# Optimization experiments

Measured on AMD Instinct MI355X. Metric: run time of the kernel, lower is better.

Reference implementation:

```python
import jax, jax.numpy as jnp
import numpy as np
from jax import lax

B, N, C, HEADS = 4096, 49, 256, 8
HD = C // HEADS
SCALE = HD ** -0.5
BRANCHES = [(1, 0), (2, 0), (3, 1), (4, 2)]  # (dilation, padding) for d1..d4


def setup_inputs() -> dict:
    key = jax.random.key(0)
    ks = jax.random.split(key, 24)
    f = lambda i, shape: jax.random.normal(ks[i], shape, dtype=jnp.float32) * 0.05
    inp = {"x": jax.random.normal(ks[0], (B, N, C), dtype=jnp.float32)}
    inp["wq"] = f(1, (C, C)); inp["bq"] = f(2, (C,))
    for j in range(4):
        inp[f"wd{j+1}"] = f(3 + 4 * j, (C, 1, 3, 3))
        inp[f"bd{j+1}"] = f(4 + 4 * j, (C,))
        inp[f"wp{j+1}"] = f(5 + 4 * j, (2 * C, C))
        inp[f"bp{j+1}"] = f(6 + 4 * j, (2 * C,))
    inp["wproj"] = f(19, (C, C)); inp["bproj"] = f(20, (C,))
    return inp


def _branch(x4, wd, bd, wp, bp, dil, pad):
    # depthwise 3x3 stride-2 dilated conv
    d = lax.conv_general_dilated(
        x4, wd, window_strides=(2, 2), padding=[(pad, pad), (pad, pad)],
        rhs_dilation=(dil, dil), dimension_numbers=('NCHW', 'OIHW', 'NCHW'),
        feature_group_count=C) + bd[None, :, None, None]
    # pointwise 1x1 conv C -> 2C
    p = jnp.einsum('oc,bchw->bohw', wp, d) + bp[None, :, None, None]
    # replicate torch's reshape(B,C,-1).permute(0,2,1).reshape(B,-1,2,h,hd).permute(2,0,3,1,4)
    p = p.reshape(B, C, -1).transpose(0, 2, 1)
    p = p.reshape(B, -1, 2, HEADS, HD).transpose(2, 0, 3, 1, 4)
    return p[0], p[1]  # k, v: (B, HEADS, hw, HD)


def _forward(x, wq, bq, wd1, bd1, wp1, bp1, wd2, bd2, wp2, bp2,
             wd3, bd3, wp3, bp3, wd4, bd4, wp4, bp4, wproj, bproj):
    H = int(N ** 0.5)
    x4 = x.transpose(0, 2, 1).reshape(B, C, H, H)
    params = [(wd1, bd1, wp1, bp1), (wd2, bd2, wp2, bp2),
              (wd3, bd3, wp3, bp3), (wd4, bd4, wp4, bp4)]
    ks_, vs_ = [], []
    for (wd, bd, wp, bp), (dil, pad) in zip(params, BRANCHES):
        k_, v_ = _branch(x4, wd, bd, wp, bp, dil, pad)
        ks_.append(k_); vs_.append(v_)
    k = jnp.concatenate(ks_, axis=2)  # (B, HEADS, 21, HD)
    v = jnp.concatenate(vs_, axis=2)
    q = (jnp.einsum('bnc,oc->bno', x, wq) + bq)
    q = q.reshape(B, N, HEADS, HD).transpose(0, 2, 1, 3) * SCALE  # (B, H, N, HD)
    attn = jax.nn.softmax(jnp.einsum('bhnd,bhmd->bhnm', q, k), axis=-1)
    out = jnp.einsum('bhnm,bhmd->bhnd', attn, v)
    out = out.transpose(0, 2, 1, 3).reshape(B, N, C)
    return jnp.einsum('bnc,oc->bno', out, wproj) + bproj


def reference(x, wq, bq, wd1, bd1, wp1, bp1, wd2, bd2, wp2, bp2,
              wd3, bd3, wp3, bp3, wd4, bd4, wp4, bp4, wproj, bproj):
    return _forward(x, wq, bq, wd1, bd1, wp1, bp1, wd2, bd2, wp2, bp2,
                    wd3, bd3, wp3, bp3, wd4, bd4, wp4, bp4, wproj, bproj)
```

## Files before the change

### kernel.cpp

```cpp
#include <hip/hip_runtime.h>
#include <stdint.h>

typedef __attribute__((ext_vector_type(8))) short bf16x8;
typedef __attribute__((ext_vector_type(8))) unsigned short u16x8;
typedef __attribute__((ext_vector_type(4))) float f32x4;

#define DEV __device__ __forceinline__

constexpr size_t WQ_PK    = 0;
constexpr size_t WPROJ_PK = 65536;
constexpr size_t WP_PK    = 131072;
constexpr size_t KVBUF    = 655360;

constexpr float SCALE_Q = 0.17677669529663687f;

DEV uint16_t f2bf(float f){
  uint32_t u = __builtin_bit_cast(uint32_t, f);
  u += 0x7fffu + ((u >> 16) & 1u);
  return (uint16_t)(u >> 16);
}

DEV u16x8 extract_par(u16x8 a, u16x8 b, uint32_t sel){
  union U { u16x8 v; uint32_t d[4]; } A, B, R;
  A.v = a; B.v = b;
  R.d[0] = __builtin_amdgcn_perm(A.d[1], A.d[0], sel);
  R.d[1] = __builtin_amdgcn_perm(A.d[3], A.d[2], sel);
  R.d[2] = __builtin_amdgcn_perm(B.d[1], B.d[0], sel);
  R.d[3] = __builtin_amdgcn_perm(B.d[3], B.d[2], sel);
  return R.v;
}

__global__ __launch_bounds__(256) void k_prepack(
    const float* __restrict__ wq,  const float* __restrict__ wp1,
    const float* __restrict__ wp2, const float* __restrict__ wp3,
    const float* __restrict__ wp4, const float* __restrict__ wproj,
    uint16_t* __restrict__ ws)
{
  int f = blockIdx.x * 256 + threadIdx.x;
  const float* src; uint16_t* dst; int g;
  if (f < 8192)       { src = wq;    dst = ws + WQ_PK;    g = f; }
  else if (f < 16384) { src = wproj; dst = ws + WPROJ_PK; g = f - 8192; }
  else {
    int j = (f - 16384) >> 14;
    src = j == 0 ? wp1 : j == 1 ? wp2 : j == 2 ? wp3 : wp4;
    dst = ws + WP_PK + (size_t)j * 131072;
    g = (f - 16384) & 16383;
  }
  int l = g & 63, kt = (g >> 6) & 7, nt = g >> 9;
  int n  = nt * 16 + (l & 15);
  int k0 = kt * 32 + (l >> 4) * 8;
  const float* s = src + (size_t)n * 256 + k0;
  u16x8 v;
  #pragma unroll
  for (int j = 0; j < 8; ++j) v[j] = f2bf(s[j]);
  *reinterpret_cast<u16x8*>(dst + (size_t)g * 8) = v;
}

__global__ __launch_bounds__(512, 2) void k_kv(
    const float* __restrict__ x,
    const float* __restrict__ wd1, const float* __restrict__ bd1, const float* __restrict__ bp1,
    const float* __restrict__ wd2, const float* __restrict__ bd2, const float* __restrict__ bp2,
    const float* __restrict__ wd3, const float* __restrict__ bd3, const float* __restrict__ bp3,
    const float* __restrict__ wd4, const float* __restrict__ bd4, const float* __restrict__ bp4,
    const uint16_t* __restrict__ ws, uint16_t* __restrict__ kvbuf)
{
  extern __shared__ char smem[];
  const int t = threadIdx.x, lane = t & 63, w = t >> 6;
  const int b0 = blockIdx.x * 8;

  constexpr int DILA[4] = {1,2,3,4}, PADA[4] = {0,0,1,2}, OWA[4] = {3,2,2,2};
  constexpr int HWA[4]  = {9,4,4,4}, OFFA[4] = {0,9,13,17}, MTA[4] = {5,2,2,2};

  {
    const int c = t & 255, half = t >> 8;
    for (int pass = 0; pass < 4; ++pass){
      const int bh = pass * 2 + half;
      float xr[49];
      #pragma unroll
      for (int p = 0; p < 49; ++p)
        xr[p] = x[((size_t)(b0 + bh) * 49 + p) * 256 + c];
      #pragma unroll
      for (int j = 0; j < 4; ++j){
        const float* wdp = j==0?wd1:j==1?wd2:j==2?wd3:wd4;
        const float* bdp = j==0?bd1:j==1?bd2:j==2?bd3:bd4;
        float wv[9];
        #pragma unroll
        for (int q = 0; q < 9; ++q) wv[q] = wdp[c * 9 + q];
        const float bdv = bdp[c];
        #pragma unroll
        for (int oy = 0; oy < OWA[j]; ++oy)
        #pragma unroll
        for (int ox = 0; ox < OWA[j]; ++ox){
          float acc = bdv;
          #pragma unroll
          for (int ky = 0; ky < 3; ++ky){
            const int yy = oy * 2 - PADA[j] + ky * DILA[j];
            if (yy < 0 || yy > 6) continue;
            #pragma unroll
            for (int kx = 0; kx < 3; ++kx){
              const int xx = ox * 2 - PADA[j] + kx * DILA[j];
              if (xx < 0 || xx > 6) continue;
              acc += xr[yy * 7 + xx] * wv[ky * 3 + kx];
            }
          }
          const int row = bh * 21 + OFFA[j] + oy * OWA[j] + ox;
          *reinterpret_cast<uint16_t*>(smem + ((row * 512 + c * 2) ^ ((row & 7) << 4))) = f2bf(acc);
        }
      }
    }
  }
  __syncthreads();

  #pragma unroll
  for (int j = 0; j < 4; ++j){
    const uint16_t* pk = ws + WP_PK + (size_t)j * 131072;
    const float* bpp = j==0?bp1:j==1?bp2:j==2?bp3:bp4;
    const int hw = HWA[j], off = OFFA[j], MV = hw * 8;
    float bpv[4];
    #pragma unroll
    for (int nt = 0; nt < 4; ++nt) bpv[nt] = bpp[w * 64 + nt * 16 + (lane & 15)];
    for (int mt = 0; mt < MTA[j]; ++mt){
      f32x4 acc[4] = {};
      const int mrow = mt * 16 + (lane & 15);
      const bool av = mrow < MV;
      const int bh = mrow / hw, s = mrow - bh * hw;
      const int arow = bh * 21 + off + s;
      const int abase = arow * 512 + (lane >> 4) * 16;
      #pragma unroll
      for (int kt = 0; kt < 8; ++kt){
        bf16x8 a = {};
        if (av) a = *reinterpret_cast<const bf16x8*>(smem + ((abase + kt * 64) ^ ((arow & 7) << 4)));
        #pragma unroll
        for (int nt = 0; nt < 4; ++nt){
          const int ntg = w * 4 + nt;
          bf16x8 bfr = *reinterpret_cast<const bf16x8*>(pk + (size_t)((ntg * 8 + kt) * 64 + lane) * 8);
          acc[nt] = __builtin_amdgcn_mfma_f32_16x16x32_bf16(a, bfr, acc[nt], 0, 0, 0);
        }
      }
      const int mr2 = mt * 16 + (lane >> 4) * 4;
      #pragma unroll
      for (int i = 0; i < 4; ++i){
        const int m = mr2 + i;
        if (m >= MV) continue;
        const int bh2 = m / hw, s2 = m - bh2 * hw;
        const size_t grow = ((size_t)(b0 + bh2) * 21 + off + s2) * 512;
        #pragma unroll
        for (int nt = 0; nt < 4; ++nt)
          kvbuf[grow + w * 64 + nt * 16 + (lane & 15)] = f2bf(acc[nt][i] + bpv[nt]);
      }
    }
  }
}

__global__ __launch_bounds__(512, 4) void k_attn(
    const float* __restrict__ x, const float* __restrict__ bq,
    const float* __restrict__ bproj, const uint16_t* __restrict__ ws,
    float* __restrict__ out)
{
  extern __shared__ char smem[];
  constexpr int OSB = 32768;
  const int t = threadIdx.x, lane = t & 63, w = t >> 6;
  const size_t b = blockIdx.x;
  const uint16_t* wq_pk    = ws + WQ_PK;
  const uint16_t* wproj_pk = ws + WPROJ_PK;
  const uint16_t* kvbuf    = ws + KVBUF;

  {
    const int r = t >> 3, c0 = (t & 7) * 32;
    u16x8 vv[4] = {};
    if (r < 49){
      const float* src = x + (b * 49 + r) * 256 + c0;
      #pragma unroll
      for (int jj = 0; jj < 4; ++jj){
        f32x4 f0 = *reinterpret_cast<const f32x4*>(src + jj * 8);
        f32x4 f1 = *reinterpret_cast<const f32x4*>(src + jj * 8 + 4);
        union { u16x8 v; uint32_t d[4]; } R;
        asm("v_cvt_pk_bf16_f32 %0, %1, %2" : "=v"(R.d[0]) : "v"(f0[0]), "v"(f0[1]));
        asm("v_cvt_pk_bf16_f32 %0, %1, %2" : "=v"(R.d[1]) : "v"(f0[2]), "v"(f0[3]));
        asm("v_cvt_pk_bf16_f32 %0, %1, %2" : "=v"(R.d[2]) : "v"(f1[0]), "v"(f1[1]));
        asm("v_cvt_pk_bf16_f32 %0, %1, %2" : "=v"(R.d[3]) : "v"(f1[2]), "v"(f1[3]));
        vv[jj] = R.v;
      }
    }
    #pragma unroll
    for (int jj = 0; jj < 4; ++jj)
      *reinterpret_cast<u16x8*>(smem + ((r * 512 + c0 * 2 + jj * 16) ^ ((r & 7) << 4))) = vv[jj];
  }

  const int sh4 = t >> 7, m = (t >> 2) & 31, dch = (t & 3) * 8;
  const bool mv = m < 21;
  uint32_t selK = 0x05040100u, selV = 0x05040100u;
  const uint16_t *rk = kvbuf, *rv = kvbuf;
  if (mv){
    int off, hw;
    if (m < 9)       { off = 0;  hw = 9; }
    else if (m < 13) { off = 9;  hw = 4; }
    else if (m < 17) { off = 13; hw = 4; }
    else             { off = 17; hw = 4; }
    const int ml = m - off;
    const int c2k = 2 * ml,     ek = c2k >= hw ? 1 : 0, sk = c2k - ek * hw;
    const int c2v = 2 * ml + 1, ev = c2v >= hw ? 1 : 0, sv = c2v - ev * hw;
    selK = ek ? 0x07060302u : 0x05040100u;
    selV = ev ? 0x07060302u : 0x05040100u;
    const int o0 = 2 * (sh4 * 32 + dch);
    rk = kvbuf + (b * 21 + off + sk) * 512 + o0;
    rv = kvbuf + (b * 21 + off + sv) * 512 + o0;
  }
  u16x8 L0 = {}, L1 = {}, L2 = {}, L3 = {};
  if (mv){
    L0 = *reinterpret_cast<const u16x8*>(rk);
    L1 = *reinterpret_cast<const u16x8*>(rk + 8);
    L2 = *reinterpret_cast<const u16x8*>(rv);
    L3 = *reinterpret_cast<const u16x8*>(rv + 8);
  }
  __syncthreads();

  f32x4 qacc[4][2] = {};
  #pragma unroll 2
  for (int kt = 0; kt < 8; ++kt){
    bf16x8 a[4];
    #pragma unroll
    for (int mt = 0; mt < 4; ++mt){
      const int row = mt * 16 + (lane & 15);
      a[mt] = *reinterpret_cast<const bf16x8*>(smem + ((row * 512 + kt * 64 + (lane >> 4) * 16) ^ ((row & 7) << 4)));
    }
    #pragma unroll
    for (int nt = 0; nt < 2; ++nt){
      bf16x8 bfr = *reinterpret_cast<const bf16x8*>(wq_pk + (size_t)(((w * 2 + nt) * 8 + kt) * 64 + lane) * 8);
      #pragma unroll
      for (int mt = 0; mt < 4; ++mt)
        qacc[mt][nt] = __builtin_amdgcn_mfma_f32_16x16x32_bf16(a[mt], bfr, qacc[mt][nt], 0, 0, 0);
    }
  }
  #pragma unroll
  for (int nt = 0; nt < 2; ++nt){
    const int col = w * 32 + nt * 16 + (lane & 15);
    const float bqv = bq[col];
    #pragma unroll
    for (int mt = 0; mt < 4; ++mt)
      #pragma unroll
      for (int i = 0; i < 4; ++i){
        const int row = mt * 16 + (lane >> 4) * 4 + i;
        *reinterpret_cast<uint16_t*>(smem + OSB + ((row * 512 + col * 2) ^ ((row & 7) << 4)))
          = f2bf((qacc[mt][nt][i] + bqv) * SCALE_Q);
      }
  }
  __syncthreads();

  for (int p = 0; p < 2; ++p){
    {
      u16x8 kf = extract_par(L0, L1, selK);
      u16x8 vf = extract_par(L2, L3, selV);
      *reinterpret_cast<u16x8*>(smem + sh4 * 2048 + ((m * 64 + dch * 2) ^ ((m & 7) << 4))) = kf;
      #pragma unroll
      for (int jj = 0; jj < 8; ++jj){
        const int d = dch + jj;
        *reinterpret_cast<uint16_t*>(smem + 8192 + sh4 * 2048 + ((d * 64 + m * 2) ^ ((d & 7) << 4))) = vf[jj];
      }
      if (p == 0 && mv){
        L0 = *reinterpret_cast<const u16x8*>(rk + 256);
        L1 = *reinterpret_cast<const u16x8*>(rk + 264);
        L2 = *reinterpret_cast<const u16x8*>(rv + 256);
        L3 = *reinterpret_cast<const u16x8*>(rv + 264);
      }
    }
    __syncthreads();

    const int h4 = w >> 1, wh = w & 1;
    const int hcol = (p * 4 + h4) * 64;
    const int pabase = 16384 + h4 * 4096;

    bf16x8 bk[2];
    #pragma unroll
    for (int nt = 0; nt < 2; ++nt){
      const int m0 = nt * 16 + (lane & 15);
      bk[nt] = *reinterpret_cast<const bf16x8*>(smem + h4 * 2048 + ((m0 * 64 + (lane >> 4) * 16) ^ ((m0 & 7) << 4)));
    }
    f32x4 sacc[2][2];
    #pragma unroll
    for (int mt = 0; mt < 2; ++mt){
      const int row = wh * 32 + mt * 16 + (lane & 15);
      bf16x8 aq = *reinterpret_cast<const bf16x8*>(smem + OSB + ((row * 512 + hcol + (lane >> 4) * 16) ^ ((row & 7) << 4)));
      #pragma unroll
      for (int nt = 0; nt < 2; ++nt){
        f32x4 z = {};
        sacc[mt][nt] = __builtin_amdgcn_mfma_f32_16x16x32_bf16(aq, bk[nt], z, 0, 0, 0);
      }
    }
    const bool ok1 = (lane & 15) < 5;
    #pragma unroll
    for (int mt = 0; mt < 2; ++mt)
      #pragma unroll
      for (int i = 0; i < 4; ++i){
        const float s0 = sacc[mt][0][i];
        const float s1 = sacc[mt][1][i];
        float mx = fmaxf(s0, ok1 ? s1 : -3.0e38f);
        #pragma unroll
        for (int dd = 1; dd < 16; dd <<= 1) mx = fmaxf(mx, __shfl_xor(mx, dd));
        const float e0 = __expf(s0 - mx);
        const float e1 = ok1 ? __expf(s1 - mx) : 0.f;
        float sm = e0 + e1;
        #pragma unroll
        for (int dd = 1; dd < 16; dd <<= 1) sm += __shfl_xor(sm, dd);
        const float inv = 1.0f / sm;
        const int pr = wh * 32 + mt * 16 + (lane >> 4) * 4 + i;
        const int c0 = lane & 15;
        *reinterpret_cast<uint16_t*>(smem + pabase + ((pr * 64 + c0 * 2) ^ ((pr & 7) << 4))) = f2bf(e0 * inv);
        *reinterpret_cast<uint16_t*>(smem + pabase + ((pr * 64 + (c0 + 16) * 2) ^ ((pr & 7) << 4))) = f2bf(e1 * inv);
      }
    f32x4 oacc[2][2];
    #pragma unroll
    for (int mt = 0; mt < 2; ++mt){
      const int pr = wh * 32 + mt * 16 + (lane & 15);
      bf16x8 ap = *reinterpret_cast<const bf16x8*>(smem + pabase + ((pr * 64 + (lane >> 4) * 16) ^ ((pr & 7) << 4)));
      #pragma unroll
      for (int nt = 0; nt < 2; ++nt){
        const int d0 = nt * 16 + (lane & 15);
        bf16x8 bv = *reinterpret_cast<const bf16x8*>(smem + 8192 + h4 * 2048 + ((d0 * 64 + (lane >> 4) * 16) ^ ((d0 & 7) << 4)));
        f32x4 z = {};
        oacc[mt][nt] = __builtin_amdgcn_mfma_f32_16x16x32_bf16(ap, bv, z, 0, 0, 0);
      }
    }
    #pragma unroll
    for (int mt = 0; mt < 2; ++mt)
      #pragma unroll
      for (int nt = 0; nt < 2; ++nt)
        #pragma unroll
        for (int i = 0; i < 4; ++i){
          const int row = wh * 32 + mt * 16 + (lane >> 4) * 4 + i;
          const int colb = hcol + (nt * 16 + (lane & 15)) * 2;
          *reinterpret_cast<uint16_t*>(smem + OSB + ((row * 512 + colb) ^ ((row & 7) << 4))) = f2bf(oacc[mt][nt][i]);
        }
    __syncthreads();
  }

  f32x4 pacc[4][2] = {};
  #pragma unroll 2
  for (int kt = 0; kt < 8; ++kt){
    bf16x8 a[4];
    #pragma unroll
    for (int mt = 0; mt < 4; ++mt){
      const int row = mt * 16 + (lane & 15);
      a[mt] = *reinterpret_cast<const bf16x8*>(smem + OSB + ((row * 512 + kt * 64 + (lane >> 4) * 16) ^ ((row & 7) << 4)));
    }
    #pragma unroll
    for (int nt = 0; nt < 2; ++nt){
      bf16x8 bfr = *reinterpret_cast<const bf16x8*>(wproj_pk + (size_t)(((w * 2 + nt) * 8 + kt) * 64 + lane) * 8);
      #pragma unroll
      for (int mt = 0; mt < 4; ++mt)
        pacc[mt][nt] = __builtin_amdgcn_mfma_f32_16x16x32_bf16(a[mt], bfr, pacc[mt][nt], 0, 0, 0);
    }
  }
  #pragma unroll
  for (int nt = 0; nt < 2; ++nt){
    const int col = w * 32 + nt * 16 + (lane & 15);
    const float bpv = bproj[col];
    #pragma unroll
    for (int mt = 0; mt < 4; ++mt)
      #pragma unroll
      for (int i = 0; i < 4; ++i){
        const int n = mt * 16 + (lane >> 4) * 4 + i;
        if (n < 49)
          out[(b * 49 + n) * 256 + col] = pacc[mt][nt][i] + bpv;
      }
  }
}

extern "C" void kernel_launch(void* const* d_in, const int* in_sizes, int n_in,
                              void* d_out, int out_size, void* d_ws, size_t ws_size,
                              hipStream_t stream)
{
  const float* x     = (const float*)d_in[0];
  const float* wq    = (const float*)d_in[1];
  const float* bq    = (const float*)d_in[2];
  const float* wd1   = (const float*)d_in[3];
  const float* bd1   = (const float*)d_in[4];
  const float* wp1   = (const float*)d_in[5];
  const float* bp1   = (const float*)d_in[6];
  const float* wd2   = (const float*)d_in[7];
  const float* bd2   = (const float*)d_in[8];
  const float* wp2   = (const float*)d_in[9];
  const float* bp2   = (const float*)d_in[10];
  const float* wd3   = (const float*)d_in[11];
  const float* bd3   = (const float*)d_in[12];
  const float* wp3   = (const float*)d_in[13];
  const float* bp3   = (const float*)d_in[14];
  const float* wd4   = (const float*)d_in[15];
  const float* bd4   = (const float*)d_in[16];
  const float* wp4   = (const float*)d_in[17];
  const float* bp4   = (const float*)d_in[18];
  const float* wproj = (const float*)d_in[19];
  const float* bproj = (const float*)d_in[20];
  uint16_t* ws = (uint16_t*)d_ws;
  float* out = (float*)d_out;

  k_prepack<<<320, 256, 0, stream>>>(wq, wp1, wp2, wp3, wp4, wproj, ws);
  k_kv<<<512, 512, 86016, stream>>>(x, wd1, bd1, bp1, wd2, bd2, bp2,
                                    wd3, bd3, bp3, wd4, bd4, bp4,
                                    ws, ws + KVBUF);
  k_attn<<<4096, 512, 65536, stream>>>(x, bq, bproj, ws, out);
}
```

Measured before the change: 277.5 us.

## Swap MFMA operand roles so outputs land channel-contiguous for vector stores

Transposes the three GEMMs (pointwise KV, Q projection, output projection): weights become the A operand and activations the B operand. Each lane's four accumulator values then sit on consecutive output channels, so results are written as packed bf16 pairs or float4 vectors instead of scattered scalar stores. Bias is loaded as a float4 per lane, and the x staging into shared memory is moved after the KV global loads so more loads are in flight. The intent is to cut store instruction count and uncoalesced global writes, at the cost of retouching index math in several stages.

```diff
diff --git a/kernel.cpp b/kernel.cpp
--- a/kernel.cpp
+++ b/kernel.cpp
@@ -4,6 +4,7 @@
 typedef __attribute__((ext_vector_type(8))) short bf16x8;
 typedef __attribute__((ext_vector_type(8))) unsigned short u16x8;
 typedef __attribute__((ext_vector_type(4))) float f32x4;
+typedef __attribute__((ext_vector_type(2))) uint32_t u32x2;
 
 #define DEV __device__ __forceinline__
 
@@ -12,12 +13,18 @@
 constexpr size_t WP_PK    = 131072;
 constexpr size_t KVBUF    = 655360;
 
-constexpr float SCALE_Q = 0.17677669529663687f;
+constexpr float SCALE_Q  = 0.17677669529663687f;
 
 DEV uint16_t f2bf(float f){
   uint32_t u = __builtin_bit_cast(uint32_t, f);
   u += 0x7fffu + ((u >> 16) & 1u);
   return (uint16_t)(u >> 16);
+}
+
+DEV uint32_t cvtpk(float a, float b){
+  uint32_t r;
+  asm("v_cvt_pk_bf16_f32 %0, %1, %2" : "=v"(r) : "v"(a), "v"(b));
+  return r;
 }
 
 DEV u16x8 extract_par(u16x8 a, u16x8 b, uint32_t sel){
@@ -66,6 +73,7 @@
 {
   extern __shared__ char smem[];
   const int t = threadIdx.x, lane = t & 63, w = t >> 6;
+  const int q4 = lane >> 4, c15 = lane & 15;
   const int b0 = blockIdx.x * 8;
 
   constexpr int DILA[4] = {1,2,3,4}, PADA[4] = {0,0,1,2}, OWA[4] = {3,2,2,2};
@@ -115,38 +123,34 @@
   for (int j = 0; j < 4; ++j){
     const uint16_t* pk = ws + WP_PK + (size_t)j * 131072;
     const float* bpp = j==0?bp1:j==1?bp2:j==2?bp3:bp4;
-    const int hw = HWA[j], off = OFFA[j], MV = hw * 8;
-    float bpv[4];
-    #pragma unroll
-    for (int nt = 0; nt < 4; ++nt) bpv[nt] = bpp[w * 64 + nt * 16 + (lane & 15)];
-    for (int mt = 0; mt < MTA[j]; ++mt){
+    const int hw = HWA[j], off = OFFA[j], MV = hw * 8, ST = MTA[j];
+    for (int st = 0; st < ST; ++st){
+      const int sl = st * 16 + c15;
+      const bool sv = sl < MV;
+      const int svc = sv ? sl : 0;
+      const int bh = svc / hw, sp = svc - bh * hw;
+      const int arow = bh * 21 + off + sp;
       f32x4 acc[4] = {};
-      const int mrow = mt * 16 + (lane & 15);
-      const bool av = mrow < MV;
-      const int bh = mrow / hw, s = mrow - bh * hw;
-      const int arow = bh * 21 + off + s;
-      const int abase = arow * 512 + (lane >> 4) * 16;
       #pragma unroll
       for (int kt = 0; kt < 8; ++kt){
-        bf16x8 a = {};
-        if (av) a = *reinterpret_cast<const bf16x8*>(smem + ((abase + kt * 64) ^ ((arow & 7) << 4)));
-        #pragma unroll
-        for (int nt = 0; nt < 4; ++nt){
-          const int ntg = w * 4 + nt;
-          bf16x8 bfr = *reinterpret_cast<const bf16x8*>(pk + (size_t)((ntg * 8 + kt) * 64 + lane) * 8);
-          acc[nt] = __builtin_amdgcn_mfma_f32_16x16x32_bf16(a, bfr, acc[nt], 0, 0, 0);
+        bf16x8 bfr = *reinterpret_cast<const bf16x8*>(smem + ((arow * 512 + kt * 64 + q4 * 16) ^ ((arow & 7) << 4)));
+        #pragma unroll
+        for (int ot = 0; ot < 4; ++ot){
+          bf16x8 aw = *reinterpret_cast<const bf16x8*>(pk + (size_t)(((w * 4 + ot) * 8 + kt) * 64 + lane) * 8);
+          acc[ot] = __builtin_amdgcn_mfma_f32_16x16x32_bf16(aw, bfr, acc[ot], 0, 0, 0);
         }
       }
-      const int mr2 = mt * 16 + (lane >> 4) * 4;
-      #pragma unroll
-      for (int i = 0; i < 4; ++i){
-        const int m = mr2 + i;
-        if (m >= MV) continue;
-        const int bh2 = m / hw, s2 = m - bh2 * hw;
-        const size_t grow = ((size_t)(b0 + bh2) * 21 + off + s2) * 512;
-        #pragma unroll
-        for (int nt = 0; nt < 4; ++nt)
-          kvbuf[grow + w * 64 + nt * 16 + (lane & 15)] = f2bf(acc[nt][i] + bpv[nt]);
+      if (sv){
+        const size_t grow = ((size_t)(b0 + bh) * 21 + off + sp) * 512;
+        #pragma unroll
+        for (int ot = 0; ot < 4; ++ot){
+          const int ob = w * 64 + ot * 16 + q4 * 4;
+          const f32x4 vb = *reinterpret_cast<const f32x4*>(bpp + ob);
+          u32x2 pkv;
+          pkv[0] = cvtpk(acc[ot][0] + vb[0], acc[ot][1] + vb[1]);
+          pkv[1] = cvtpk(acc[ot][2] + vb[2], acc[ot][3] + vb[3]);
+          *reinterpret_cast<u32x2*>(kvbuf + grow + ob) = pkv;
+        }
       }
     }
   }
@@ -160,32 +164,11 @@
   extern __shared__ char smem[];
   constexpr int OSB = 32768;
   const int t = threadIdx.x, lane = t & 63, w = t >> 6;
+  const int q4 = lane >> 4, c15 = lane & 15;
   const size_t b = blockIdx.x;
   const uint16_t* wq_pk    = ws + WQ_PK;
   const uint16_t* wproj_pk = ws + WPROJ_PK;
   const uint16_t* kvbuf    = ws + KVBUF;
-
-  {
-    const int r = t >> 3, c0 = (t & 7) * 32;
-    u16x8 vv[4] = {};
-    if (r < 49){
-      const float* src = x + (b * 49 + r) * 256 + c0;
-      #pragma unroll
-      for (int jj = 0; jj < 4; ++jj){
-        f32x4 f0 = *reinterpret_cast<const f32x4*>(src + jj * 8);
-        f32x4 f1 = *reinterpret_cast<const f32x4*>(src + jj * 8 + 4);
-        union { u16x8 v; uint32_t d[4]; } R;
-        asm("v_cvt_pk_bf16_f32 %0, %1, %2" : "=v"(R.d[0]) : "v"(f0[0]), "v"(f0[1]));
-        asm("v_cvt_pk_bf16_f32 %0, %1, %2" : "=v"(R.d[1]) : "v"(f0[2]), "v"(f0[3]));
-        asm("v_cvt_pk_bf16_f32 %0, %1, %2" : "=v"(R.d[2]) : "v"(f1[0]), "v"(f1[1]));
-        asm("v_cvt_pk_bf16_f32 %0, %1, %2" : "=v"(R.d[3]) : "v"(f1[2]), "v"(f1[3]));
-        vv[jj] = R.v;
-      }
-    }
-    #pragma unroll
-    for (int jj = 0; jj < 4; ++jj)
-      *reinterpret_cast<u16x8*>(smem + ((r * 512 + c0 * 2 + jj * 16) ^ ((r & 7) << 4))) = vv[jj];
-  }
 
   const int sh4 = t >> 7, m = (t >> 2) & 31, dch = (t & 3) * 8;
   const bool mv = m < 21;
@@ -213,37 +196,59 @@
     L2 = *reinterpret_cast<const u16x8*>(rv);
     L3 = *reinterpret_cast<const u16x8*>(rv + 8);
   }
+
+  {
+    const int r = t >> 3, c0 = (t & 7) * 32;
+    u16x8 vv[4] = {};
+    if (r < 49){
+      const float* src = x + (b * 49 + r) * 256 + c0;
+      #pragma unroll
+      for (int jj = 0; jj < 4; ++jj){
+        f32x4 f0 = *reinterpret_cast<const f32x4*>(src + jj * 8);
+        f32x4 f1 = *reinterpret_cast<const f32x4*>(src + jj * 8 + 4);
+        union { u16x8 v; uint32_t d[4]; } R;
+        R.d[0] = cvtpk(f0[0], f0[1]);
+        R.d[1] = cvtpk(f0[2], f0[3]);
+        R.d[2] = cvtpk(f1[0], f1[1]);
+        R.d[3] = cvtpk(f1[2], f1[3]);
+        vv[jj] = R.v;
+      }
+    }
+    #pragma unroll
+    for (int jj = 0; jj < 4; ++jj)
+      *reinterpret_cast<u16x8*>(smem + ((r * 512 + c0 * 2 + jj * 16) ^ ((r & 7) << 4))) = vv[jj];
+  }
   __syncthreads();
 
-  f32x4 qacc[4][2] = {};
+  f32x4 qacc[2][4] = {};
   #pragma unroll 2
   for (int kt = 0; kt < 8; ++kt){
-    bf16x8 a[4];
-    #pragma unroll
-    for (int mt = 0; mt < 4; ++mt){
-      const int row = mt * 16 + (lane & 15);
-      a[mt] = *reinterpret_cast<const bf16x8*>(smem + ((row * 512 + kt * 64 + (lane >> 4) * 16) ^ ((row & 7) << 4)));
-    }
-    #pragma unroll
-    for (int nt = 0; nt < 2; ++nt){
-      bf16x8 bfr = *reinterpret_cast<const bf16x8*>(wq_pk + (size_t)(((w * 2 + nt) * 8 + kt) * 64 + lane) * 8);
-      #pragma unroll
-      for (int mt = 0; mt < 4; ++mt)
-        qacc[mt][nt] = __builtin_amdgcn_mfma_f32_16x16x32_bf16(a[mt], bfr, qacc[mt][nt], 0, 0, 0);
+    bf16x8 bx[4];
+    #pragma unroll
+    for (int nt = 0; nt < 4; ++nt){
+      const int row = nt * 16 + c15;
+      bx[nt] = *reinterpret_cast<const bf16x8*>(smem + ((row * 512 + kt * 64 + q4 * 16) ^ ((row & 7) << 4)));
+    }
+    #pragma unroll
+    for (int mt = 0; mt < 2; ++mt){
+      bf16x8 aw = *reinterpret_cast<const bf16x8*>(wq_pk + (size_t)(((w * 2 + mt) * 8 + kt) * 64 + lane) * 8);
+      #pragma unroll
+      for (int nt = 0; nt < 4; ++nt)
+        qacc[mt][nt] = __builtin_amdgcn_mfma_f32_16x16x32_bf16(aw, bx[nt], qacc[mt][nt], 0, 0, 0);
     }
   }
   #pragma unroll
-  for (int nt = 0; nt < 2; ++nt){
-    const int col = w * 32 + nt * 16 + (lane & 15);
-    const float bqv = bq[col];
-    #pragma unroll
-    for (int mt = 0; mt < 4; ++mt)
-      #pragma unroll
-      for (int i = 0; i < 4; ++i){
-        const int row = mt * 16 + (lane >> 4) * 4 + i;
-        *reinterpret_cast<uint16_t*>(smem + OSB + ((row * 512 + col * 2) ^ ((row & 7) << 4)))
-          = f2bf((qacc[mt][nt][i] + bqv) * SCALE_Q);
-      }
+  for (int mt = 0; mt < 2; ++mt){
+    const int ob = w * 32 + mt * 16 + q4 * 4;
+    const f32x4 vb = *reinterpret_cast<const f32x4*>(bq + ob);
+    #pragma unroll
+    for (int nt = 0; nt < 4; ++nt){
+      const int row = nt * 16 + c15;
+      u32x2 pkq;
+      pkq[0] = cvtpk((qacc[mt][nt][0] + vb[0]) * SCALE_Q, (qacc[mt][nt][1] + vb[1]) * SCALE_Q);
+      pkq[1] = cvtpk((qacc[mt][nt][2] + vb[2]) * SCALE_Q, (qacc[mt][nt][3] + vb[3]) * SCALE_Q);
+      *reinterpret_cast<u32x2*>(smem + OSB + ((row * 512 + ob * 2) ^ ((row & 7) << 4))) = pkq;
+    }
   }
   __syncthreads();
 
@@ -273,21 +278,21 @@
     bf16x8 bk[2];
     #pragma unroll
     for (int nt = 0; nt < 2; ++nt){
-      const int m0 = nt * 16 + (lane & 15);
-      bk[nt] = *reinterpret_cast<const bf16x8*>(smem + h4 * 2048 + ((m0 * 64 + (lane >> 4) * 16) ^ ((m0 & 7) << 4)));
+      const int m0 = nt * 16 + c15;
+      bk[nt] = *reinterpret_cast<const bf16x8*>(smem + h4 * 2048 + ((m0 * 64 + q4 * 16) ^ ((m0 & 7) << 4)));
     }
     f32x4 sacc[2][2];
     #pragma unroll
     for (int mt = 0; mt < 2; ++mt){
-      const int row = wh * 32 + mt * 16 + (lane & 15);
-      bf16x8 aq = *reinterpret_cast<const bf16x8*>(smem + OSB + ((row * 512 + hcol + (lane >> 4) * 16) ^ ((row & 7) << 4)));
+      const int row = wh * 32 + mt * 16 + c15;
+      bf16x8 aq = *reinterpret_cast<const bf16x8*>(smem + OSB + ((row * 512 + hcol + q4 * 16) ^ ((row & 7) << 4)));
       #pragma unroll
       for (int nt = 0; nt < 2; ++nt){
         f32x4 z = {};
         sacc[mt][nt] = __builtin_amdgcn_mfma_f32_16x16x32_bf16(aq, bk[nt], z, 0, 0, 0);
       }
     }
-    const bool ok1 = (lane & 15) < 5;
+    const bool ok1 = c15 < 5;
     #pragma unroll
     for (int mt = 0; mt < 2; ++mt)
       #pragma unroll
@@ -303,20 +308,19 @@
         #pragma unroll
         for (int dd = 1; dd < 16; dd <<= 1) sm += __shfl_xor(sm, dd);
         const float inv = 1.0f / sm;
-        const int pr = wh * 32 + mt * 16 + (lane >> 4) * 4 + i;
-        const int c0 = lane & 15;
-        *reinterpret_cast<uint16_t*>(smem + pabase + ((pr * 64 + c0 * 2) ^ ((pr & 7) << 4))) = f2bf(e0 * inv);
-        *reinterpret_cast<uint16_t*>(smem + pabase + ((pr * 64 + (c0 + 16) * 2) ^ ((pr & 7) << 4))) = f2bf(e1 * inv);
+        const int pr = wh * 32 + mt * 16 + q4 * 4 + i;
+        *reinterpret_cast<uint16_t*>(smem + pabase + ((pr * 64 + c15 * 2) ^ ((pr & 7) << 4))) = f2bf(e0 * inv);
+        *reinterpret_cast<uint16_t*>(smem + pabase + ((pr * 64 + (c15 + 16) * 2) ^ ((pr & 7) << 4))) = f2bf(e1 * inv);
       }
     f32x4 oacc[2][2];
     #pragma unroll
     for (int mt = 0; mt < 2; ++mt){
-      const int pr = wh * 32 + mt * 16 + (lane & 15);
-      bf16x8 ap = *reinterpret_cast<const bf16x8*>(smem + pabase + ((pr * 64 + (lane >> 4) * 16) ^ ((pr & 7) << 4)));
+      const int pr = wh * 32 + mt * 16 + c15;
+      bf16x8 ap = *reinterpret_cast<const bf16x8*>(smem + pabase + ((pr * 64 + q4 * 16) ^ ((pr & 7) << 4)));
       #pragma unroll
       for (int nt = 0; nt < 2; ++nt){
-        const int d0 = nt * 16 + (lane & 15);
-        bf16x8 bv = *reinterpret_cast<const bf16x8*>(smem + 8192 + h4 * 2048 + ((d0 * 64 + (lane >> 4) * 16) ^ ((d0 & 7) << 4)));
+        const int d0 = nt * 16 + c15;
+        bf16x8 bv = *reinterpret_cast<const bf16x8*>(smem + 8192 + h4 * 2048 + ((d0 * 64 + q4 * 16) ^ ((d0 & 7) << 4)));
         f32x4 z = {};
         oacc[mt][nt] = __builtin_amdgcn_mfma_f32_16x16x32_bf16(ap, bv, z, 0, 0, 0);
       }
@@ -327,42 +331,40 @@
       for (int nt = 0; nt < 2; ++nt)
         #pragma unroll
         for (int i = 0; i < 4; ++i){
-          const int row = wh * 32 + mt * 16 + (lane >> 4) * 4 + i;
-          const int colb = hcol + (nt * 16 + (lane & 15)) * 2;
+          const int row = wh * 32 + mt * 16 + q4 * 4 + i;
+          const int colb = hcol + (nt * 16 + c15) * 2;
           *reinterpret_cast<uint16_t*>(smem + OSB + ((row * 512 + colb) ^ ((row & 7) << 4))) = f2bf(oacc[mt][nt][i]);
         }
     __syncthreads();
   }
 
-  f32x4 pacc[4][2] = {};
+  f32x4 pacc[2][4] = {};
   #pragma unroll 2
   for (int kt = 0; kt < 8; ++kt){
-    bf16x8 a[4];
-    #pragma unroll
-    for (int mt = 0; mt < 4; ++mt){
-      const int row = mt * 16 + (lane & 15);
-      a[mt] = *reinterpret_cast<const bf16x8*>(smem + OSB + ((row * 512 + kt * 64 + (lane >> 4) * 16) ^ ((row & 7) << 4)));
-    }
-    #pragma unroll
-    for (int nt = 0; nt < 2; ++nt){
-      bf16x8 bfr = *reinterpret_cast<const bf16x8*>(wproj_pk + (size_t)(((w * 2 + nt) * 8 + kt) * 64 + lane) * 8);
-      #pragma unroll
-      for (int mt = 0; mt < 4; ++mt)
-        pacc[mt][nt] = __builtin_amdgcn_mfma_f32_16x16x32_bf16(a[mt], bfr, pacc[mt][nt], 0, 0, 0);
+    bf16x8 bo[4];
+    #pragma unroll
+    for (int nt = 0; nt < 4; ++nt){
+      const int row = nt * 16 + c15;
+      bo[nt] = *reinterpret_cast<const bf16x8*>(smem + OSB + ((row * 512 + kt * 64 + q4 * 16) ^ ((row & 7) << 4)));
+    }
+    #pragma unroll
+    for (int mt = 0; mt < 2; ++mt){
+      bf16x8 aw = *reinterpret_cast<const bf16x8*>(wproj_pk + (size_t)(((w * 2 + mt) * 8 + kt) * 64 + lane) * 8);
+      #pragma unroll
+      for (int nt = 0; nt < 4; ++nt)
+        pacc[mt][nt] = __builtin_amdgcn_mfma_f32_16x16x32_bf16(aw, bo[nt], pacc[mt][nt], 0, 0, 0);
     }
   }
   #pragma unroll
-  for (int nt = 0; nt < 2; ++nt){
-    const int col = w * 32 + nt * 16 + (lane & 15);
-    const float bpv = bproj[col];
-    #pragma unroll
-    for (int mt = 0; mt < 4; ++mt)
-      #pragma unroll
-      for (int i = 0; i < 4; ++i){
-        const int n = mt * 16 + (lane >> 4) * 4 + i;
-        if (n < 49)
-          out[(b * 49 + n) * 256 + col] = pacc[mt][nt][i] + bpv;
-      }
+  for (int mt = 0; mt < 2; ++mt){
+    const int ob = w * 32 + mt * 16 + q4 * 4;
+    const f32x4 vb = *reinterpret_cast<const f32x4*>(bproj + ob);
+    #pragma unroll
+    for (int nt = 0; nt < 4; ++nt){
+      const int n = nt * 16 + c15;
+      if (n < 49)
+        *reinterpret_cast<f32x4*>(out + (b * 49 + n) * 256 + ob) = pacc[mt][nt] + vb;
+    }
   }
 }
 
```

Result: slower. 329.8 us (+18.9%).
